# Kernel tuning notes

Measured on AMD Instinct MI355X. Metric: run time of the kernel, lower is better.

The kernel has to match this reference:

```python
import jax, jax.numpy as jnp
import numpy as np

B, S, D = 2, 2048, 2048
H = 16
HD = D // H            # 128 head dim
L = 512                # latent dim
R = 64                 # rope dim (min(64, HD) = 64)
RH = R // 2
SCALE = HD ** -0.5     # note: uses head_dim, not head_dim+rope_dim
NEG = jnp.float32(-1e9)


def _rope_tables():
    inv_freq = 1.0 / (10000.0 ** (jnp.arange(0, R, 2, dtype=jnp.float32) / R))  # [RH]
    pos = jnp.arange(S, dtype=jnp.float32)
    freqs = pos[:, None] * inv_freq[None, :]  # [S, RH]
    return jnp.cos(freqs), jnp.sin(freqs)


def _apply_rope(x, cos, sin):
    # x: [B, H, S, R], interleaved even/odd rotation as in the torch source
    xe, xo = x[..., 0::2], x[..., 1::2]                    # [B,H,S,RH]
    c = cos[None, None]
    s = sin[None, None]
    re = xe * c - xo * s
    ro = xe * s + xo * c
    return jnp.stack([re, ro], axis=-1).reshape(x.shape)   # re-interleave


def setup_inputs() -> dict:
    key = jax.random.key(0)
    ks = jax.random.split(key, 8)
    std = 0.02
    f32 = jnp.float32
    return {
        "x":     jax.random.normal(ks[0], (B, S, D), f32),
        "W_ckv": jax.random.normal(ks[1], (D, L), f32) * std,      # compress_kv
        "W_kv":  jax.random.normal(ks[2], (L, 2 * D), f32) * std,  # kv_proj
        "W_cq":  jax.random.normal(ks[3], (D, L), f32) * std,      # compress_q
        "W_q":   jax.random.normal(ks[4], (L, D), f32) * std,      # q_proj
        "W_qr":  jax.random.normal(ks[5], (L, H * R), f32) * std,  # q_rope
        "W_kr":  jax.random.normal(ks[6], (L, R), f32) * std,      # k_rope
        "W_out": jax.random.normal(ks[7], (D, D), f32) * std,      # out_proj
    }


def reference(x, W_ckv, W_kv, W_cq, W_q, W_qr, W_kr, W_out):
    cos, sin = _rope_tables()

    c_kv = x @ W_ckv                                   # [B,S,L]
    kv = c_kv @ W_kv                                   # [B,S,2D]
    c_q = x @ W_cq                                     # [B,S,L]

    q_c = (c_q @ W_q).reshape(B, S, H, HD).transpose(0, 2, 1, 3)    # [B,H,S,HD]
    q_r = (c_q @ W_qr).reshape(B, S, H, R).transpose(0, 2, 1, 3)    # [B,H,S,R]
    k_r = (c_kv @ W_kr)[:, None, :, :]                               # [B,1,S,R]

    k_c, v = jnp.split(kv, 2, axis=-1)
    k_c = k_c.reshape(B, S, H, HD).transpose(0, 2, 1, 3)             # [B,H,S,HD]
    v = v.reshape(B, S, H, HD).transpose(0, 2, 1, 3)                 # [B,H,S,HD]

    q_r = _apply_rope(q_r, cos, sin)
    k_r = jnp.broadcast_to(_apply_rope(k_r, cos, sin), (B, H, S, R))

    q = jnp.concatenate([q_c, q_r], axis=-1)                         # [B,H,S,HD+R]
    k = jnp.concatenate([k_c, k_r], axis=-1)                         # [B,H,S,HD+R]

    scores = jnp.einsum("bhqd,bhkd->bhqk", q, k) * SCALE             # [B,H,S,S]
    causal = jnp.tril(jnp.ones((S, S), dtype=bool))
    scores = jnp.where(causal[None, None], scores, NEG)
    p = jax.nn.softmax(scores, axis=-1)
    attended = jnp.einsum("bhqk,bhkd->bhqd", p, v)                   # [B,H,S,HD]

    out = attended.transpose(0, 2, 1, 3).reshape(B, S, D) @ W_out    # [B,S,D]
    return out  # dropout is identity in eval / p=0
```

## Files before the change

kernel.cpp:

```cpp
#include <hip/hip_runtime.h>
#include <hip/hip_bf16.h>
#include <cstdint>
#include <cstddef>

typedef __bf16 bf16;
typedef __attribute__((ext_vector_type(2))) __bf16 bf16x2;
typedef __attribute__((ext_vector_type(4))) __bf16 bf16x4;
typedef __attribute__((ext_vector_type(8))) __bf16 bf16x8;
typedef __attribute__((ext_vector_type(4))) float f32x4;

#define MFMA16(a, b, c) __builtin_amdgcn_mfma_f32_16x16x32_bf16((a), (b), (c), 0, 0, 0)
#define SCALE_L2E 0.127517432f

#define QCR_STRIDE 3072
#define KV_STRIDE  4160

__device__ __forceinline__ void gload16(const void* g, void* l) {
    __builtin_amdgcn_global_load_lds(
        (const __attribute__((address_space(1))) void*)g,
        (__attribute__((address_space(3))) void*)l, 16, 0, 0);
}

__device__ __forceinline__ void bar_lgkm() {
    asm volatile("s_waitcnt lgkmcnt(0)" ::: "memory");
    __builtin_amdgcn_s_barrier();
    asm volatile("" ::: "memory");
}

__device__ __forceinline__ int pack_bf16(float a, float b) {
    bf16x2 p; p[0] = (bf16)a; p[1] = (bf16)b;
    return __builtin_bit_cast(int, p);
}

__global__ void k_cvt(const float* __restrict__ in, bf16* __restrict__ out, int n4)
{
    int i = blockIdx.x * blockDim.x + threadIdx.x;
    int stride = gridDim.x * blockDim.x;
    const float4* in4 = (const float4*)in;
    bf16x4* o4 = (bf16x4*)out;
    for (; i < n4; i += stride) {
        float4 v = in4[i];
        bf16x4 o;
        o[0] = (bf16)v.x; o[1] = (bf16)v.y; o[2] = (bf16)v.z; o[3] = (bf16)v.w;
        o4[i] = o;
    }
}

__global__ __launch_bounds__(256) void k_cvtT(const float* __restrict__ in,
                                              bf16* __restrict__ out, int Kd, int Nd)
{
    __shared__ float tile[32][33];
    const int k0 = blockIdx.y * 32, n0 = blockIdx.x * 32;
    const int t = threadIdx.x;
    const int r = t >> 3, c4 = (t & 7) * 4;
    float4 v = *(const float4*)(in + (size_t)(k0 + r) * Nd + n0 + c4);
    tile[r][c4 + 0] = v.x; tile[r][c4 + 1] = v.y;
    tile[r][c4 + 2] = v.z; tile[r][c4 + 3] = v.w;
    __syncthreads();
    bf16x4 o;
    o[0] = (bf16)tile[c4 + 0][r]; o[1] = (bf16)tile[c4 + 1][r];
    o[2] = (bf16)tile[c4 + 2][r]; o[3] = (bf16)tile[c4 + 3][r];
    *(bf16x4*)(out + (size_t)(n0 + r) * Kd + k0 + c4) = o;
}

__global__ __launch_bounds__(256) void k_cvtT6(
    const float* __restrict__ w_ckv, const float* __restrict__ w_kv,
    const float* __restrict__ w_cq, const float* __restrict__ w_q,
    const float* __restrict__ w_qr, const float* __restrict__ w_kr,
    bf16* __restrict__ WCT, bf16* __restrict__ WKVKRT, bf16* __restrict__ WQQRT)
{
    __shared__ float tile[32][33];
    int bid = blockIdx.x;
    const float* src; bf16* dst; int Kd, Nd, loc;
    if (bid < 1024)      { src = w_ckv; dst = WCT;                   Kd = 2048; Nd = 512;  loc = bid; }
    else if (bid < 3072) { src = w_kv;  dst = WKVKRT;                Kd = 512;  Nd = 4096; loc = bid - 1024; }
    else if (bid < 4096) { src = w_cq;  dst = WCT + 512ull * 2048;   Kd = 2048; Nd = 512;  loc = bid - 3072; }
    else if (bid < 5120) { src = w_q;   dst = WQQRT;                 Kd = 512;  Nd = 2048; loc = bid - 4096; }
    else if (bid < 5632) { src = w_qr;  dst = WQQRT + 2048ull * 512; Kd = 512;  Nd = 1024; loc = bid - 5120; }
    else                 { src = w_kr;  dst = WKVKRT + 4096ull * 512; Kd = 512; Nd = 64;   loc = bid - 5632; }
    const int nbx = Nd / 32;
    const int n0 = (loc % nbx) * 32, k0 = (loc / nbx) * 32;
    const int t = threadIdx.x;
    const int r = t >> 3, c4 = (t & 7) * 4;
    float4 v = *(const float4*)(src + (size_t)(k0 + r) * Nd + n0 + c4);
    tile[r][c4 + 0] = v.x; tile[r][c4 + 1] = v.y;
    tile[r][c4 + 2] = v.z; tile[r][c4 + 3] = v.w;
    __syncthreads();
    bf16x4 o;
    o[0] = (bf16)tile[c4 + 0][r]; o[1] = (bf16)tile[c4 + 1][r];
    o[2] = (bf16)tile[c4 + 2][r]; o[3] = (bf16)tile[c4 + 3][r];
    *(bf16x4*)(dst + (size_t)(n0 + r) * Kd + k0 + c4) = o;
}

template<int MF, int NF, bool F32OUT>
__device__ __forceinline__ void gemm_body(
    const bf16* __restrict__ A, const bf16* __restrict__ BT,
    bf16* __restrict__ Cb, float* __restrict__ Cf,
    int M, int N, int K, int lda, float cscale, int bx, int by,
    bf16* As, bf16* Bs)
{
    constexpr int ASTR = MF * 1024, BSTR = NF * 1024;
    const int t = threadIdx.x;
    const int m0 = by * (MF * 32);
    const int n0 = bx * (NF * 32);
    const int wid = t >> 6, lane = t & 63;
    const int wm = (wid >> 1) * (MF * 16), wn = (wid & 1) * (NF * 16);
    const int lr = lane & 15, lk = (lane >> 4) * 8;

    const int srow = t >> 2, skc = (t & 3) << 3;
    const int bn0 = min(n0 + srow, N - 1);
    const int bn1 = min(n0 + srow + 64, N - 1);

    f32x4 acc[MF][NF];
    const f32x4 z = {0.f, 0.f, 0.f, 0.f};
#pragma unroll
    for (int m = 0; m < MF; ++m)
#pragma unroll
        for (int n = 0; n < NF; ++n) acc[m][n] = z;

    auto stage = [&](int buf, int k0) {
        gload16(BT + (size_t)bn0 * K + k0 + skc, Bs + buf * BSTR + t * 8);
        if constexpr (NF == 4)
            gload16(BT + (size_t)bn1 * K + k0 + skc, Bs + buf * BSTR + (t + 256) * 8);
        gload16(A + (size_t)(m0 + srow) * lda + k0 + skc, As + buf * ASTR + t * 8);
        if constexpr (MF == 4)
            gload16(A + (size_t)(m0 + srow + 64) * lda + k0 + skc, As + buf * ASTR + (t + 256) * 8);
    };

    stage(0, 0);
    __syncthreads();

    for (int k0 = 0; k0 < K; k0 += 32) {
        const int cur = (k0 >> 5) & 1;
        if (k0 + 32 < K) stage(cur ^ 1, k0 + 32);

        bf16x8 af[MF], bfr[NF];
#pragma unroll
        for (int m = 0; m < MF; ++m)
            af[m] = *(const bf16x8*)(As + cur * ASTR + (wm + m * 16 + lr) * 32 + lk);
#pragma unroll
        for (int n = 0; n < NF; ++n)
            bfr[n] = *(const bf16x8*)(Bs + cur * BSTR + (wn + n * 16 + lr) * 32 + lk);
#pragma unroll
        for (int m = 0; m < MF; ++m)
#pragma unroll
            for (int n = 0; n < NF; ++n)
                acc[m][n] = MFMA16(af[m], bfr[n], acc[m][n]);

        __syncthreads();
    }

    const int lrow4 = (lane >> 4) * 4;
#pragma unroll
    for (int m = 0; m < MF; ++m)
#pragma unroll
        for (int n = 0; n < NF; ++n)
#pragma unroll
            for (int i = 0; i < 4; ++i) {
                int r = m0 + wm + m * 16 + lrow4 + i;
                int c = n0 + wn + n * 16 + lr;
                if (r < M && c < N) {
                    float val = acc[m][n][i] * cscale;
                    if constexpr (F32OUT) Cf[(size_t)r * N + c] = val;
                    else Cb[(size_t)r * N + c] = (bf16)val;
                }
            }
}

template<int MF, int NF, bool F32OUT>
__global__ __launch_bounds__(256) void k_gemm_bt(
    const bf16* __restrict__ A, const bf16* __restrict__ BT,
    bf16* __restrict__ Cb, float* __restrict__ Cf,
    int M, int N, int K, int lda, float cscale)
{
    __shared__ bf16 As[2 * MF * 1024];
    __shared__ bf16 Bs[2 * NF * 1024];
    gemm_body<MF, NF, F32OUT>(A, BT, Cb, Cf, M, N, K, lda, cscale,
                              blockIdx.x, blockIdx.y, As, Bs);
}

__global__ __launch_bounds__(256) void k_gemm_dual(
    const bf16* __restrict__ C, const bf16* __restrict__ WKVKRT,
    const bf16* __restrict__ WQQRT, bf16* __restrict__ KVKR, bf16* __restrict__ QCR)
{
    __shared__ bf16 As[2 * 4096];
    __shared__ bf16 Bs[2 * 4096];
    int bid = blockIdx.x;
    if (bid < 1056) {
        gemm_body<4, 4, false>(C, WKVKRT, KVKR, nullptr, 4096, 4160, 512, 1024,
                               1.0f, bid % 33, bid / 33, As, Bs);
    } else {
        bid -= 1056;
        gemm_body<4, 4, false>(C + 512, WQQRT, QCR, nullptr, 4096, 3072, 512, 1024,
                               SCALE_L2E, bid % 24, bid / 24, As, Bs);
    }
}

__global__ void k_rope(bf16* __restrict__ qcr, bf16* __restrict__ kvkr)
{
    const int bid = blockIdx.x;
    const int t = threadIdx.x;
    if (bid < 8192) {
        int idx = bid * 256 + t;
        int row = idx >> 9;
        int rem = idx & 511;
        int h = rem >> 5;
        int i = rem & 31;
        int s = row & 2047;
        float ang = (float)s * __expf(-(float)i * 0.28782313662f);
        float c = cosf(ang), sn = sinf(ang);
        size_t base = (size_t)row * QCR_STRIDE + 2048 + h * 64 + (i << 1);
        float xe = (float)qcr[base], xo = (float)qcr[base + 1];
        qcr[base] = (bf16)(xe * c - xo * sn);
        qcr[base + 1] = (bf16)(xe * sn + xo * c);
    } else {
        int idx = (bid - 8192) * 256 + t;
        int row = idx >> 5;
        int i = idx & 31;
        int s = row & 2047;
        float ang = (float)s * __expf(-(float)i * 0.28782313662f);
        float c = cosf(ang), sn = sinf(ang);
        size_t base = (size_t)row * KV_STRIDE + 4096 + (i << 1);
        float xe = (float)kvkr[base], xo = (float)kvkr[base + 1];
        kvkr[base] = (bf16)(xe * c - xo * sn);
        kvkr[base + 1] = (bf16)(xe * sn + xo * c);
    }
}

__global__ __launch_bounds__(256, 3) void k_attn(
    const bf16* __restrict__ qcr, const bf16* __restrict__ kvkr,
    bf16* __restrict__ att)
{
    __shared__ bf16 Ksc[64 * 128];
    __shared__ bf16 Ksr[64 * 64];
    __shared__ bf16 Vt[128 * 64];

    const int L = blockIdx.x;
    const int qt = 31 - (L >> 5);
    const int bh = L & 31;
    const int h = bh & 15, b = bh >> 4;

    const int t = threadIdx.x;
    const int wid = t >> 6, lane = t & 63;
    const int lr = lane & 15, lq = lane >> 4, lk = lq * 8;
    const size_t rowbase = (size_t)b * 2048;

    const f32x4 z = {0.f, 0.f, 0.f, 0.f};

    auto rho = [](int r) {
        return (((r >> 5) & 1) << 5) | (((r >> 2) & 1) << 4) | (((r >> 3) & 3) << 2) | (r & 3);
    };

    const int vk = (t & 31) * 2;
    const int vf = (t >> 5) * 8;

    bf16x8 rc[4], rr[2], rv[4];
    auto LOAD = [&](int kb) {
#pragma unroll
        for (int i = 0; i < 4; ++i) {
            int bb = t + 256 * i;
            int row = bb >> 4, gcb = bb & 15;
            rc[i] = *(const bf16x8*)(kvkr + (rowbase + kb + row) * KV_STRIDE + h * 128 + gcb * 8);
        }
#pragma unroll
        for (int i = 0; i < 2; ++i) {
            int bb = t + 256 * i;
            int row = bb >> 3, gcb = bb & 7;
            rr[i] = *(const bf16x8*)(kvkr + (rowbase + kb + row) * KV_STRIDE + 4096 + gcb * 8);
        }
#pragma unroll
        for (int i = 0; i < 2; ++i) {
            const bf16* vs = kvkr + (rowbase + kb + vk) * KV_STRIDE + 2048 + h * 128 + vf + 64 * i;
            rv[2 * i]     = *(const bf16x8*)vs;
            rv[2 * i + 1] = *(const bf16x8*)(vs + KV_STRIDE);
        }
    };
    auto WRITE = [&]() {
#pragma unroll
        for (int i = 0; i < 4; ++i) {
            int bb = t + 256 * i;
            int row = rho(bb >> 4), gcb = bb & 15;
            int scb = (gcb & 8) | ((gcb ^ row) & 7);
            *(bf16x8*)(Ksc + row * 128 + scb * 8) = rc[i];
        }
#pragma unroll
        for (int i = 0; i < 2; ++i) {
            int bb = t + 256 * i;
            int row = rho(bb >> 3), gcb = bb & 7;
            int scb = (gcb ^ row) & 7;
            *(bf16x8*)(Ksr + row * 64 + scb * 8) = rr[i];
        }
#pragma unroll
        for (int i = 0; i < 2; ++i)
#pragma unroll
            for (int j = 0; j < 8; ++j) {
                int feat = vf + 64 * i + j;
                int scb = ((vk >> 3) ^ (feat & 7)) & 7;
                bf16x2 pr; pr[0] = rv[2 * i][j]; pr[1] = rv[2 * i + 1][j];
                *(bf16x2*)(Vt + feat * 64 + scb * 8 + (vk & 7)) = pr;
            }
    };

    const int qrow_w = qt * 64 + wid * 16;
    const int qi = qrow_w + lr;

    bf16x8 qf[6];
    {
        const size_t qrow = rowbase + qi;
        const bf16* qp = qcr + qrow * QCR_STRIDE + h * 128;
#pragma unroll
        for (int ks = 0; ks < 4; ++ks) qf[ks] = *(const bf16x8*)(qp + ks * 32 + lk);
        const bf16* qp2 = qcr + qrow * QCR_STRIDE + 2048 + h * 64;
#pragma unroll
        for (int ks = 0; ks < 2; ++ks) qf[4 + ks] = *(const bf16x8*)(qp2 + ks * 32 + lk);
    }

    float mrow = -3e38f, lsum = 0.f;
    f32x4 o[8];
#pragma unroll
    for (int n = 0; n < 8; ++n) o[n] = z;

    const int nkt = qt + 1;
    LOAD(0);

#pragma unroll 1
    for (int kt = 0; kt < nkt; ++kt) {
        const int kb = kt * 64;
        bar_lgkm();
        WRITE();
        if (kt + 1 < nkt) LOAD(kb + 64);
        bar_lgkm();

        if (kb > qrow_w + 15) continue;

        f32x4 sacc[4];
#pragma unroll
        for (int kg = 0; kg < 4; ++kg) {
            f32x4 s = z;
            const int key = kg * 16 + lr;
#pragma unroll
            for (int ks = 0; ks < 4; ++ks) {
                int cb = ks * 4 + lq;
                int scb = (cb & 8) | ((cb ^ key) & 7);
                bf16x8 kf = *(const bf16x8*)(Ksc + key * 128 + scb * 8);
                s = MFMA16(kf, qf[ks], s);
            }
#pragma unroll
            for (int ks = 0; ks < 2; ++ks) {
                int cb = ks * 4 + lq;
                int scb = (cb ^ key) & 7;
                bf16x8 kf = *(const bf16x8*)(Ksr + key * 64 + scb * 8);
                s = MFMA16(kf, qf[4 + ks], s);
            }
            sacc[kg] = s;
        }

        const bool domask = (kb + 63) > qrow_w;
        if (domask) {
#pragma unroll
            for (int kg = 0; kg < 4; ++kg) {
                int keybase = kb + ((kg >> 1) << 5) + (lq << 3) + ((kg & 1) << 2);
#pragma unroll
                for (int i = 0; i < 4; ++i)
                    if (keybase + i > qi) sacc[kg][i] = -3e38f;
            }
        }

        f32x4 mv;
#pragma unroll
        for (int i = 0; i < 4; ++i)
            mv[i] = fmaxf(fmaxf(sacc[0][i], sacc[1][i]), fmaxf(sacc[2][i], sacc[3][i]));
        float mx = fmaxf(fmaxf(mv[0], mv[1]), fmaxf(mv[2], mv[3]));
        mx = fmaxf(mx, __shfl_xor(mx, 16, 64));
        mx = fmaxf(mx, __shfl_xor(mx, 32, 64));

        if (__any(mx > mrow)) {
            float mnew = fmaxf(mrow, mx);
            float scl = __builtin_amdgcn_exp2f(mrow - mnew);
            mrow = mnew;
            lsum *= scl;
#pragma unroll
            for (int n = 0; n < 8; ++n)
#pragma unroll
                for (int i = 0; i < 4; ++i) o[n][i] *= scl;
        }

        f32x4 sv = z;
#pragma unroll
        for (int kg = 0; kg < 4; ++kg)
#pragma unroll
            for (int i = 0; i < 4; ++i) {
                float pv = __builtin_amdgcn_exp2f(sacc[kg][i] - mrow);
                sacc[kg][i] = pv;
                sv[i] += pv;
            }
        float rs = (sv[0] + sv[1]) + (sv[2] + sv[3]);
        rs += __shfl_xor(rs, 16, 64);
        rs += __shfl_xor(rs, 32, 64);
        lsum += rs;

#pragma unroll
        for (int s = 0; s < 2; ++s) {
            union { int4 iv; bf16x8 v; } pb;
            pb.iv.x = pack_bf16(sacc[2 * s][0], sacc[2 * s][1]);
            pb.iv.y = pack_bf16(sacc[2 * s][2], sacc[2 * s][3]);
            pb.iv.z = pack_bf16(sacc[2 * s + 1][0], sacc[2 * s + 1][1]);
            pb.iv.w = pack_bf16(sacc[2 * s + 1][2], sacc[2 * s + 1][3]);
#pragma unroll
            for (int n = 0; n < 8; ++n) {
                int feat = n * 16 + lr;
                int scb = ((s * 4 + lq) ^ (feat & 7)) & 7;
                bf16x8 vfr = *(const bf16x8*)(Vt + feat * 64 + scb * 8);
                o[n] = MFMA16(vfr, pb.v, o[n]);
            }
        }
    }

    const float inv = 1.f / lsum;
    const size_t orow = (rowbase + qi) * 2048 + h * 128;
#pragma unroll
    for (int n = 0; n < 8; ++n) {
        bf16x4 ov;
#pragma unroll
        for (int i = 0; i < 4; ++i) ov[i] = (bf16)(o[n][i] * inv);
        *(bf16x4*)(att + orow + n * 16 + (lq << 2)) = ov;
    }
}

extern "C" void kernel_launch(void* const* d_in, const int* in_sizes, int n_in,
                              void* d_out, int out_size, void* d_ws, size_t ws_size,
                              hipStream_t stream)
{
    (void)in_sizes; (void)n_in; (void)out_size; (void)ws_size;
    const float* x = (const float*)d_in[0];
    const float* w_ckv = (const float*)d_in[1];
    const float* w_kv = (const float*)d_in[2];
    const float* w_cq = (const float*)d_in[3];
    const float* w_q = (const float*)d_in[4];
    const float* w_qr = (const float*)d_in[5];
    const float* w_kr = (const float*)d_in[6];
    const float* w_out = (const float*)d_in[7];
    float* out = (float*)d_out;

    char* ws = (char*)d_ws;
    size_t off = 0;
    auto take = [&](size_t elems) -> bf16* {
        bf16* p = (bf16*)(ws + off);
        off += (elems * sizeof(bf16) + 255) & ~(size_t)255;
        return p;
    };
    bf16* WCT    = take(1024ull * 2048);
    bf16* WKVKRT = take(4160ull * 512);
    bf16* WQQRT  = take(3072ull * 512);
    bf16* C      = take(4096ull * 1024);
    bf16* KVKR   = take(4096ull * 4160);
    bf16* QCR    = take(4096ull * 3072);
    bf16* ATT    = take(4096ull * 2048);
    bf16* WOUTT  = C;
    bf16* XB     = KVKR;

    k_cvtT6<<<5664, 256, 0, stream>>>(w_ckv, w_kv, w_cq, w_q, w_qr, w_kr,
                                      WCT, WKVKRT, WQQRT);

    k_cvt<<<2048, 256, 0, stream>>>(x, XB, (4096 * 2048) / 4);

    k_gemm_bt<4, 2, false><<<dim3(16, 32), 256, 0, stream>>>(
        XB, WCT, C, nullptr, 4096, 1024, 2048, 2048, 1.0f);

    k_gemm_dual<<<1824, 256, 0, stream>>>(C, WKVKRT, WQQRT, KVKR, QCR);

    k_cvtT<<<dim3(64, 64), 256, 0, stream>>>(w_out, WOUTT, 2048, 2048);

    k_rope<<<8704, 256, 0, stream>>>(QCR, KVKR);

    k_attn<<<1024, 256, 0, stream>>>(QCR, KVKR, ATT);

    k_gemm_bt<2, 4, true><<<dim3(16, 64), 256, 0, stream>>>(
        ATT, WOUTT, nullptr, out, 4096, 2048, 2048, 2048, 1.0f);
}
```

Measured before the change: 248.3 us.

## Fuse RoPE into projection GEMM epilogue, merge convert kernels, add MFMA priority hints

Applies the rotary embedding inside the dual GEMM epilogue, using a lane shuffle to fetch the paired even/odd column, so the separate read-modify-write RoPE kernel goes away. Merges the weight-transpose and x-convert kernels into one launch. Raises wave priority around the MFMA sections of the attention kernel. These remove a kernel launch and an extra pass over QCR/KVKR, at the cost of extra sincos work in the GEMM epilogue and the lower-precision __sincosf intrinsic.

```diff
diff --git a/kernel.cpp b/kernel.cpp
--- a/kernel.cpp
+++ b/kernel.cpp
@@ -32,18 +32,48 @@
     return __builtin_bit_cast(int, p);
 }
 
-__global__ void k_cvt(const float* __restrict__ in, bf16* __restrict__ out, int n4)
-{
-    int i = blockIdx.x * blockDim.x + threadIdx.x;
-    int stride = gridDim.x * blockDim.x;
-    const float4* in4 = (const float4*)in;
-    bf16x4* o4 = (bf16x4*)out;
-    for (; i < n4; i += stride) {
-        float4 v = in4[i];
-        bf16x4 o;
-        o[0] = (bf16)v.x; o[1] = (bf16)v.y; o[2] = (bf16)v.z; o[3] = (bf16)v.w;
-        o4[i] = o;
-    }
+__global__ __launch_bounds__(256) void k_cvtAll(
+    const float* __restrict__ w_ckv, const float* __restrict__ w_kv,
+    const float* __restrict__ w_cq, const float* __restrict__ w_q,
+    const float* __restrict__ w_qr, const float* __restrict__ w_kr,
+    bf16* __restrict__ WCT, bf16* __restrict__ WKVKRT, bf16* __restrict__ WQQRT,
+    const float* __restrict__ x, bf16* __restrict__ XB)
+{
+    __shared__ float tile[32][33];
+    int bid = blockIdx.x;
+    const int t = threadIdx.x;
+    if (bid >= 5664) {
+        int n4 = (4096 * 2048) / 4;
+        int i = (bid - 5664) * 256 + t;
+        int stride = 2048 * 256;
+        const float4* in4 = (const float4*)x;
+        bf16x4* o4 = (bf16x4*)XB;
+        for (; i < n4; i += stride) {
+            float4 v = in4[i];
+            bf16x4 o;
+            o[0] = (bf16)v.x; o[1] = (bf16)v.y; o[2] = (bf16)v.z; o[3] = (bf16)v.w;
+            o4[i] = o;
+        }
+        return;
+    }
+    const float* src; bf16* dst; int Kd, Nd, loc;
+    if (bid < 1024)      { src = w_ckv; dst = WCT;                   Kd = 2048; Nd = 512;  loc = bid; }
+    else if (bid < 3072) { src = w_kv;  dst = WKVKRT;                Kd = 512;  Nd = 4096; loc = bid - 1024; }
+    else if (bid < 4096) { src = w_cq;  dst = WCT + 512ull * 2048;   Kd = 2048; Nd = 512;  loc = bid - 3072; }
+    else if (bid < 5120) { src = w_q;   dst = WQQRT;                 Kd = 512;  Nd = 2048; loc = bid - 4096; }
+    else if (bid < 5632) { src = w_qr;  dst = WQQRT + 2048ull * 512; Kd = 512;  Nd = 1024; loc = bid - 5120; }
+    else                 { src = w_kr;  dst = WKVKRT + 4096ull * 512; Kd = 512; Nd = 64;   loc = bid - 5632; }
+    const int nbx = Nd / 32;
+    const int n0 = (loc % nbx) * 32, k0 = (loc / nbx) * 32;
+    const int r = t >> 3, c4 = (t & 7) * 4;
+    float4 v = *(const float4*)(src + (size_t)(k0 + r) * Nd + n0 + c4);
+    tile[r][c4 + 0] = v.x; tile[r][c4 + 1] = v.y;
+    tile[r][c4 + 2] = v.z; tile[r][c4 + 3] = v.w;
+    __syncthreads();
+    bf16x4 o;
+    o[0] = (bf16)tile[c4 + 0][r]; o[1] = (bf16)tile[c4 + 1][r];
+    o[2] = (bf16)tile[c4 + 2][r]; o[3] = (bf16)tile[c4 + 3][r];
+    *(bf16x4*)(dst + (size_t)(n0 + r) * Kd + k0 + c4) = o;
 }
 
 __global__ __launch_bounds__(256) void k_cvtT(const float* __restrict__ in,
@@ -63,40 +93,11 @@
     *(bf16x4*)(out + (size_t)(n0 + r) * Kd + k0 + c4) = o;
 }
 
-__global__ __launch_bounds__(256) void k_cvtT6(
-    const float* __restrict__ w_ckv, const float* __restrict__ w_kv,
-    const float* __restrict__ w_cq, const float* __restrict__ w_q,
-    const float* __restrict__ w_qr, const float* __restrict__ w_kr,
-    bf16* __restrict__ WCT, bf16* __restrict__ WKVKRT, bf16* __restrict__ WQQRT)
-{
-    __shared__ float tile[32][33];
-    int bid = blockIdx.x;
-    const float* src; bf16* dst; int Kd, Nd, loc;
-    if (bid < 1024)      { src = w_ckv; dst = WCT;                   Kd = 2048; Nd = 512;  loc = bid; }
-    else if (bid < 3072) { src = w_kv;  dst = WKVKRT;                Kd = 512;  Nd = 4096; loc = bid - 1024; }
-    else if (bid < 4096) { src = w_cq;  dst = WCT + 512ull * 2048;   Kd = 2048; Nd = 512;  loc = bid - 3072; }
-    else if (bid < 5120) { src = w_q;   dst = WQQRT;                 Kd = 512;  Nd = 2048; loc = bid - 4096; }
-    else if (bid < 5632) { src = w_qr;  dst = WQQRT + 2048ull * 512; Kd = 512;  Nd = 1024; loc = bid - 5120; }
-    else                 { src = w_kr;  dst = WKVKRT + 4096ull * 512; Kd = 512; Nd = 64;   loc = bid - 5632; }
-    const int nbx = Nd / 32;
-    const int n0 = (loc % nbx) * 32, k0 = (loc / nbx) * 32;
-    const int t = threadIdx.x;
-    const int r = t >> 3, c4 = (t & 7) * 4;
-    float4 v = *(const float4*)(src + (size_t)(k0 + r) * Nd + n0 + c4);
-    tile[r][c4 + 0] = v.x; tile[r][c4 + 1] = v.y;
-    tile[r][c4 + 2] = v.z; tile[r][c4 + 3] = v.w;
-    __syncthreads();
-    bf16x4 o;
-    o[0] = (bf16)tile[c4 + 0][r]; o[1] = (bf16)tile[c4 + 1][r];
-    o[2] = (bf16)tile[c4 + 2][r]; o[3] = (bf16)tile[c4 + 3][r];
-    *(bf16x4*)(dst + (size_t)(n0 + r) * Kd + k0 + c4) = o;
-}
-
-template<int MF, int NF, bool F32OUT>
+template<int MF, int NF, bool F32OUT, bool ROPE>
 __device__ __forceinline__ void gemm_body(
     const bf16* __restrict__ A, const bf16* __restrict__ BT,
     bf16* __restrict__ Cb, float* __restrict__ Cf,
-    int M, int N, int K, int lda, float cscale, int bx, int by,
+    int M, int N, int K, int lda, float cscale, int ropeStart, int bx, int by,
     bf16* As, bf16* Bs)
 {
     constexpr int ASTR = MF * 1024, BSTR = NF * 1024;
@@ -159,8 +160,20 @@
             for (int i = 0; i < 4; ++i) {
                 int r = m0 + wm + m * 16 + lrow4 + i;
                 int c = n0 + wn + n * 16 + lr;
+                float val = acc[m][n][i] * cscale;
+                if constexpr (ROPE) {
+                    float part = __shfl_xor(val, 1, 64);
+                    if (c >= ropeStart) {
+                        int i2 = ((c - ropeStart) & 63) >> 1;
+                        int s = r & 2047;
+                        float ang = (float)s * __expf(-(float)i2 * 0.28782313662f);
+                        float sn, cs;
+                        __sincosf(ang, &sn, &cs);
+                        val = (c & 1) ? (part * sn + val * cs)
+                                      : (val * cs - part * sn);
+                    }
+                }
                 if (r < M && c < N) {
-                    float val = acc[m][n][i] * cscale;
                     if constexpr (F32OUT) Cf[(size_t)r * N + c] = val;
                     else Cb[(size_t)r * N + c] = (bf16)val;
                 }
@@ -175,8 +188,8 @@
 {
     __shared__ bf16 As[2 * MF * 1024];
     __shared__ bf16 Bs[2 * NF * 1024];
-    gemm_body<MF, NF, F32OUT>(A, BT, Cb, Cf, M, N, K, lda, cscale,
-                              blockIdx.x, blockIdx.y, As, Bs);
+    gemm_body<MF, NF, F32OUT, false>(A, BT, Cb, Cf, M, N, K, lda, cscale, 1 << 30,
+                                     blockIdx.x, blockIdx.y, As, Bs);
 }
 
 __global__ __launch_bounds__(256) void k_gemm_dual(
@@ -187,43 +200,12 @@
     __shared__ bf16 Bs[2 * 4096];
     int bid = blockIdx.x;
     if (bid < 1056) {
-        gemm_body<4, 4, false>(C, WKVKRT, KVKR, nullptr, 4096, 4160, 512, 1024,
-                               1.0f, bid % 33, bid / 33, As, Bs);
+        gemm_body<4, 4, false, true>(C, WKVKRT, KVKR, nullptr, 4096, 4160, 512, 1024,
+                                     1.0f, 4096, bid % 33, bid / 33, As, Bs);
     } else {
         bid -= 1056;
-        gemm_body<4, 4, false>(C + 512, WQQRT, QCR, nullptr, 4096, 3072, 512, 1024,
-                               SCALE_L2E, bid % 24, bid / 24, As, Bs);
-    }
-}
-
-__global__ void k_rope(bf16* __restrict__ qcr, bf16* __restrict__ kvkr)
-{
-    const int bid = blockIdx.x;
-    const int t = threadIdx.x;
-    if (bid < 8192) {
-        int idx = bid * 256 + t;
-        int row = idx >> 9;
-        int rem = idx & 511;
-        int h = rem >> 5;
-        int i = rem & 31;
-        int s = row & 2047;
-        float ang = (float)s * __expf(-(float)i * 0.28782313662f);
-        float c = cosf(ang), sn = sinf(ang);
-        size_t base = (size_t)row * QCR_STRIDE + 2048 + h * 64 + (i << 1);
-        float xe = (float)qcr[base], xo = (float)qcr[base + 1];
-        qcr[base] = (bf16)(xe * c - xo * sn);
-        qcr[base + 1] = (bf16)(xe * sn + xo * c);
-    } else {
-        int idx = (bid - 8192) * 256 + t;
-        int row = idx >> 5;
-        int i = idx & 31;
-        int s = row & 2047;
-        float ang = (float)s * __expf(-(float)i * 0.28782313662f);
-        float c = cosf(ang), sn = sinf(ang);
-        size_t base = (size_t)row * KV_STRIDE + 4096 + (i << 1);
-        float xe = (float)kvkr[base], xo = (float)kvkr[base + 1];
-        kvkr[base] = (bf16)(xe * c - xo * sn);
-        kvkr[base + 1] = (bf16)(xe * sn + xo * c);
+        gemm_body<4, 4, false, true>(C + 512, WQQRT, QCR, nullptr, 4096, 3072, 512, 1024,
+                                     SCALE_L2E, 2048, bid % 24, bid / 24, As, Bs);
     }
 }
 
@@ -334,6 +316,7 @@
         if (kb > qrow_w + 15) continue;
 
         f32x4 sacc[4];
+        __builtin_amdgcn_s_setprio(1);
 #pragma unroll
         for (int kg = 0; kg < 4; ++kg) {
             f32x4 s = z;
@@ -354,6 +337,7 @@
             }
             sacc[kg] = s;
         }
+        __builtin_amdgcn_s_setprio(0);
 
         const bool domask = (kb + 63) > qrow_w;
         if (domask) {
@@ -399,6 +383,7 @@
         rs += __shfl_xor(rs, 32, 64);
         lsum += rs;
 
+        __builtin_amdgcn_s_setprio(1);
 #pragma unroll
         for (int s = 0; s < 2; ++s) {
             union { int4 iv; bf16x8 v; } pb;
@@ -414,6 +399,7 @@
                 o[n] = MFMA16(vfr, pb.v, o[n]);
             }
         }
+        __builtin_amdgcn_s_setprio(0);
     }
 
     const float inv = 1.f / lsum;
@@ -459,10 +445,8 @@
     bf16* WOUTT  = C;
     bf16* XB     = KVKR;
 
-    k_cvtT6<<<5664, 256, 0, stream>>>(w_ckv, w_kv, w_cq, w_q, w_qr, w_kr,
-                                      WCT, WKVKRT, WQQRT);
-
-    k_cvt<<<2048, 256, 0, stream>>>(x, XB, (4096 * 2048) / 4);
+    k_cvtAll<<<7712, 256, 0, stream>>>(w_ckv, w_kv, w_cq, w_q, w_qr, w_kr,
+                                       WCT, WKVKRT, WQQRT, x, XB);
 
     k_gemm_bt<4, 2, false><<<dim3(16, 32), 256, 0, stream>>>(
         XB, WCT, C, nullptr, 4096, 1024, 2048, 2048, 1.0f);
@@ -471,8 +455,6 @@
 
     k_cvtT<<<dim3(64, 64), 256, 0, stream>>>(w_out, WOUTT, 2048, 2048);
 
-    k_rope<<<8704, 256, 0, stream>>>(QCR, KVKR);
-
     k_attn<<<1024, 256, 0, stream>>>(QCR, KVKR, ATT);
 
     k_gemm_bt<2, 4, true><<<dim3(16, 64), 256, 0, stream>>>(
```

After: 248.4 us. No clear change (+0.0%).
